# Performance work log

Measured on AMD Instinct MI355X. Metric: run time of the kernel, lower is better.

The kernel has to match this reference:

```python
import jax, jax.numpy as jnp
import numpy as np

N_HEAD, D_MODEL, D_K, D_V = 8, 512, 64, 64
LN_EPS = 1e-3


def setup_inputs() -> dict:
    key = jax.random.key(0)
    ks = jax.random.split(key, 9)
    B, L = 4, 2048
    q = jax.random.normal(ks[0], (B, L, D_MODEL), dtype=jnp.float32)
    k = jax.random.normal(ks[1], (B, L, D_MODEL), dtype=jnp.float32)
    v = jax.random.normal(ks[2], (B, L, D_MODEL), dtype=jnp.float32)
    # xavier-normal-ish init for projections
    s_qk = (2.0 / (D_MODEL + D_K)) ** 0.5
    s_v = (2.0 / (D_MODEL + D_V)) ** 0.5
    s_p = (2.0 / (N_HEAD * D_V + D_MODEL)) ** 0.5
    w_qs = jax.random.normal(ks[3], (N_HEAD, D_MODEL, D_K), dtype=jnp.float32) * s_qk
    w_ks = jax.random.normal(ks[4], (N_HEAD, D_MODEL, D_K), dtype=jnp.float32) * s_qk
    w_vs = jax.random.normal(ks[5], (N_HEAD, D_MODEL, D_V), dtype=jnp.float32) * s_v
    proj_w = jax.random.normal(ks[6], (D_MODEL, N_HEAD * D_V), dtype=jnp.float32) * s_p  # torch Linear weight (out,in)
    proj_b = jnp.zeros((D_MODEL,), dtype=jnp.float32)
    a_2 = jnp.ones((D_MODEL,), dtype=jnp.float32)
    b_2 = jnp.zeros((D_MODEL,), dtype=jnp.float32)
    return {"q": q, "k": k, "v": v, "w_qs": w_qs, "w_ks": w_ks, "w_vs": w_vs,
            "proj_w": proj_w, "proj_b": proj_b, "a_2": a_2, "b_2": b_2}


def _layer_norm(z, a_2, b_2):
    # torch.std default is unbiased (ddof=1); module divides by (sigma + eps)
    mu = jnp.mean(z, axis=-1, keepdims=True)
    sigma = jnp.std(z, axis=-1, keepdims=True, ddof=1)
    return (z - mu) / (sigma + LN_EPS) * a_2 + b_2


def reference(q, k, v, w_qs, w_ks, w_vs, proj_w, proj_b, a_2, b_2):
    B, Lq, D = q.shape
    temper = jnp.asarray(D, q.dtype) ** 0.5  # note: sqrt(d_model), as in source
    residual = q
    # per-head projections: (h, b, l, dk)
    qh = jnp.einsum('bld,hdk->hblk', q, w_qs)
    kh = jnp.einsum('bmd,hdk->hbmk', k, w_ks)
    vh = jnp.einsum('bmd,hdv->hbmv', v, w_vs)
    # full score matrix (h, b, lq, lk) -- faithful to naive bmm attention
    attn = jax.nn.softmax(jnp.einsum('hblk,hbmk->hblm', qh, kh) / temper, axis=-1)
    out = jnp.einsum('hblm,hbmv->hblv', attn, vh)          # (h, b, lq, dv)
    out = jnp.transpose(out, (1, 2, 0, 3)).reshape(B, Lq, -1)  # concat heads -> (b, lq, h*dv)
    out = out @ proj_w.T + proj_b
    out = _layer_norm(out + residual, a_2, b_2)
    attns = attn.reshape(-1, attn.shape[2], attn.shape[3])  # (h*b, lq, lk) matching torch layout
    return out, attns
```

## Files before the change

kernel.cpp:

```cpp
#include <hip/hip_runtime.h>
#include <stdint.h>

typedef unsigned short u16;
typedef u16   u16x4v __attribute__((ext_vector_type(4)));
typedef u16   u16x8v __attribute__((ext_vector_type(8)));
typedef short s16x8v __attribute__((ext_vector_type(8)));
typedef float f32x4v __attribute__((ext_vector_type(4)));

#define DEV static __device__ __forceinline__

DEV u16 f2bf(float f){
  union { float f; unsigned u; } v; v.f = f;
  unsigned r = v.u + 0x7FFFu + ((v.u >> 16) & 1u);
  return (u16)(r >> 16);
}

DEV f32x4v mfma16(s16x8v a, s16x8v b, f32x4v c){
  return __builtin_amdgcn_mfma_f32_16x16x32_bf16(a, b, c, 0, 0, 0);
}

__global__ __launch_bounds__(256) void k_wall(const float* __restrict__ w_qs,
                                              const float* __restrict__ w_ks,
                                              const float* __restrict__ w_vs,
                                              const float* __restrict__ proj_w,
                                              u16* __restrict__ wt, u16* __restrict__ wtp,
                                              float qscale){
  int gid = blockIdx.x;
  int tsel = gid >> 10;
  int e = (gid & 1023) * 256 + threadIdx.x;
  if(tsel == 3){
    wtp[e] = f2bf(proj_w[e]);
  } else {
    const float* w = tsel == 0 ? w_qs : (tsel == 1 ? w_ks : w_vs);
    float sc = tsel == 0 ? qscale : 1.0f;
    int n = e >> 9, d = e & 511;
    int h = n >> 6, kk = n & 63;
    wt[tsel * 262144 + n * 512 + d] = f2bf(w[h * 32768 + d * 64 + kk] * sc);
  }
}

__global__ __launch_bounds__(256) void k_qkv(const float* __restrict__ Q,
                                             const float* __restrict__ K,
                                             const float* __restrict__ V,
                                             const u16* __restrict__ Wt,
                                             u16* __restrict__ qhh, u16* __restrict__ khh,
                                             u16* __restrict__ vtt){
  __shared__ __align__(16) u16 Xs[32 * 520];
  const int t = threadIdx.x;
  const int lane = t & 63, w = t >> 6;
  const int g = lane >> 4, li = lane & 15;
  const int i0 = blockIdx.x * 32;
  const int y = blockIdx.y;
  const int tsel = y >> 1;
  const float* X = tsel == 0 ? Q : (tsel == 1 ? K : V);
  const int n0 = (y & 1) * 256 + w * 64;

  #pragma unroll
  for(int it = 0; it < 16; ++it){
    int s = it * 256 + t, row = s >> 7, c4 = s & 127;
    f32x4v xv = *(const f32x4v*)(X + (size_t)(i0 + row) * 512 + c4 * 4);
    u16x4v bv; bv[0]=f2bf(xv[0]); bv[1]=f2bf(xv[1]); bv[2]=f2bf(xv[2]); bv[3]=f2bf(xv[3]);
    *(u16x4v*)(Xs + row * 520 + c4 * 4) = bv;
  }
  __syncthreads();

  const int wbase = tsel * 512 + n0;
  const u16* wp0 = Wt + (size_t)(wbase +  0 + li) * 512 + g * 8;
  const u16* wp1 = Wt + (size_t)(wbase + 16 + li) * 512 + g * 8;
  const u16* wp2 = Wt + (size_t)(wbase + 32 + li) * 512 + g * 8;
  const u16* wp3 = Wt + (size_t)(wbase + 48 + li) * 512 + g * 8;

#define LOADW(S, c) { \
  S##0 = *(const s16x8v*)(wp0 + (c) * 32); \
  S##1 = *(const s16x8v*)(wp1 + (c) * 32); \
  S##2 = *(const s16x8v*)(wp2 + (c) * 32); \
  S##3 = *(const s16x8v*)(wp3 + (c) * 32); }
#define COMPW(S, c) { \
  int k0 = (c) * 32 + g * 8; \
  s16x8v a0 = *(const s16x8v*)(Xs + li * 520 + k0); \
  s16x8v a1 = *(const s16x8v*)(Xs + (16 + li) * 520 + k0); \
  acc[0][0] = mfma16(a0, S##0, acc[0][0]); acc[1][0] = mfma16(a1, S##0, acc[1][0]); \
  acc[0][1] = mfma16(a0, S##1, acc[0][1]); acc[1][1] = mfma16(a1, S##1, acc[1][1]); \
  acc[0][2] = mfma16(a0, S##2, acc[0][2]); acc[1][2] = mfma16(a1, S##2, acc[1][2]); \
  acc[0][3] = mfma16(a0, S##3, acc[0][3]); acc[1][3] = mfma16(a1, S##3, acc[1][3]); }

  f32x4v acc[2][4] = {};
  s16x8v wA0, wA1, wA2, wA3, wB0, wB1, wB2, wB3;
  LOADW(wA, 0);
  #pragma unroll
  for(int c = 0; c < 16; c += 2){
    LOADW(wB, c + 1);
    COMPW(wA, c);
    if(c + 2 < 16) LOADW(wA, c + 2);
    COMPW(wB, c + 1);
  }
#undef LOADW
#undef COMPW

  if(tsel < 2){
    u16* Y = tsel == 0 ? qhh : khh;
    #pragma unroll
    for(int rg = 0; rg < 2; ++rg)
      #pragma unroll
      for(int j = 0; j < 4; ++j){
        int n = n0 + j * 16 + li, h = n >> 6, dk = n & 63;
        #pragma unroll
        for(int r = 0; r < 4; ++r){
          int i = i0 + rg * 16 + g * 4 + r, bb = i >> 11, m = i & 2047;
          Y[((size_t)(h * 4 + bb) * 2048 + m) * 64 + dk] = f2bf(acc[rg][j][r]);
        }
      }
  } else {
    #pragma unroll
    for(int rg = 0; rg < 2; ++rg)
      #pragma unroll
      for(int j = 0; j < 4; ++j){
        int n = n0 + j * 16 + li;
        u16x4v pk;
        #pragma unroll
        for(int r = 0; r < 4; ++r) pk[r] = f2bf(acc[rg][j][r]);
        *(u16x4v*)(vtt + (size_t)n * 8192 + i0 + g * 8 + rg * 4) = pk;
      }
  }
}


#define LOADK(B, ht) { \
  const u16* _p = kp + (size_t)(ht) * 2048; \
  B##0 = *(const s16x8v*)(_p); \
  B##1 = *(const s16x8v*)(_p + 32); \
  B##2 = *(const s16x8v*)(_p + 1024); \
  B##3 = *(const s16x8v*)(_p + 1056); }

#define STEPA(B) { \
  f32x4v z0 = {}, z1 = {}; \
  z0 = mfma16(B##0, bq00, z0); z0 = mfma16(B##1, bq01, z0); \
  z1 = mfma16(B##2, bq00, z1); z1 = mfma16(B##3, bq01, z1); \
  _Pragma("unroll") for(int r = 0; r < 4; ++r){ s00[r] += exp2f(z0[r]); s01[r] += exp2f(z1[r]); } \
  f32x4v y0 = {}, y1 = {}; \
  y0 = mfma16(B##0, bq10, y0); y0 = mfma16(B##1, bq11, y0); \
  y1 = mfma16(B##2, bq10, y1); y1 = mfma16(B##3, bq11, y1); \
  _Pragma("unroll") for(int r = 0; r < 4; ++r){ s10[r] += exp2f(y0[r]); s11[r] += exp2f(y1[r]); } }

#define LOADV(B, ht) { \
  const u16* _p = vp + (ht) * 32; \
  B##0 = *(const s16x8v*)(_p); \
  B##1 = *(const s16x8v*)(_p + 131072); \
  B##2 = *(const s16x8v*)(_p + 262144); \
  B##3 = *(const s16x8v*)(_p + 393216); }

#define QS_HALF(KB, VB, bqa, bqb, lb, qs_, ht) { \
  f32x4v z0 = {}, z1 = {}; \
  z0 = mfma16(KB##0, bqa, z0); z0 = mfma16(KB##1, bqb, z0); \
  z1 = mfma16(KB##2, bqa, z1); z1 = mfma16(KB##3, bqb, z1); \
  f32x4v p0, p1; \
  _Pragma("unroll") for(int r = 0; r < 4; ++r){ p0[r] = exp2f(z0[r] + lb); p1[r] = exp2f(z1[r] + lb); } \
  float* _ab = attb + (size_t)((qs_) * 16 + li) * 2048 + (ht) * 32 + g * 4; \
  __builtin_nontemporal_store(p0, (f32x4v*)(_ab)); \
  __builtin_nontemporal_store(p1, (f32x4v*)(_ab + 16)); \
  union { u16 hh[8]; s16x8v v; } _u; \
  _Pragma("unroll") for(int r = 0; r < 4; ++r){ _u.hh[r] = f2bf(p0[r]); _u.hh[4 + r] = f2bf(p1[r]); } \
  acc##qs_##0 = mfma16(_u.v, VB##0, acc##qs_##0); \
  acc##qs_##1 = mfma16(_u.v, VB##1, acc##qs_##1); \
  acc##qs_##2 = mfma16(_u.v, VB##2, acc##qs_##2); \
  acc##qs_##3 = mfma16(_u.v, VB##3, acc##qs_##3); }

#define STEPB(KB, VB, ht) { \
  QS_HALF(KB, VB, bq00, bq01, lb0, 0, ht); \
  QS_HALF(KB, VB, bq10, bq11, lb1, 1, ht); }

__global__ __launch_bounds__(256, 3) void k_attn(const u16* __restrict__ QHH, const u16* __restrict__ KHH,
                                                 const u16* __restrict__ VTT,
                                                 u16* __restrict__ XC, float* __restrict__ ATT){
  __shared__ float Lp[2][2][32];
  __shared__ float AccS[2][32][64];
  const int t = threadIdx.x, lane = t & 63, w = t >> 6;
  const int g = lane >> 4, li = lane & 15;
  const int qs = w >> 1, mh = w & 1;
  const int gid = blockIdx.x;
  const int xcd = gid & 7, rem = gid >> 3;
  const int qt = rem & 31;
  const int hb = xcd * 4 + (rem >> 5);
  const int h = hb >> 2, b = hb & 3;
  const size_t base_hb = (size_t)hb * 2048;
  const int qbase = qt * 64 + qs * 32;

  s16x8v bq00, bq01, bq10, bq11;
  {
    const u16* qp0 = QHH + (base_hb + qbase + li) * 64 + g * 8;
    const u16* qp1 = QHH + (base_hb + qbase + 16 + li) * 64 + g * 8;
    bq00 = *(const s16x8v*)(qp0); bq01 = *(const s16x8v*)(qp0 + 32);
    bq10 = *(const s16x8v*)(qp1); bq11 = *(const s16x8v*)(qp1 + 32);
  }
  const u16* kp = KHH + (base_hb + li) * 64 + g * 8 + (size_t)mh * 65536;
  const u16* vp = VTT + (size_t)(h * 64 + li) * 8192 + b * 2048 + g * 8 + mh * 1024;
  float* attb = ATT + (base_hb + qbase) * 2048 + mh * 1024;

  f32x4v s00 = {}, s01 = {}, s10 = {}, s11 = {};
  {
    s16x8v kA0, kA1, kA2, kA3, kB0, kB1, kB2, kB3;
    LOADK(kA, 0);
    for(int ht = 0; ht < 30; ht += 2){
      LOADK(kB, ht + 1);
      STEPA(kA);
      LOADK(kA, ht + 2);
      STEPA(kB);
    }
    LOADK(kB, 31);
    STEPA(kA);
    STEPA(kB);
  }
  float l0 = (s00[0]+s00[1]+s00[2]+s00[3]) + (s01[0]+s01[1]+s01[2]+s01[3]);
  float l1 = (s10[0]+s10[1]+s10[2]+s10[3]) + (s11[0]+s11[1]+s11[2]+s11[3]);
  l0 += __shfl_xor(l0, 16, 64); l0 += __shfl_xor(l0, 32, 64);
  l1 += __shfl_xor(l1, 16, 64); l1 += __shfl_xor(l1, 32, 64);
  if(lane < 16){ Lp[qs][mh][li] = l0; Lp[qs][mh][16 + li] = l1; }
  __syncthreads();
  const float lb0 = -__log2f(Lp[qs][0][li]      + Lp[qs][1][li]);
  const float lb1 = -__log2f(Lp[qs][0][16 + li] + Lp[qs][1][16 + li]);

  f32x4v acc00 = {}, acc01 = {}, acc02 = {}, acc03 = {};
  f32x4v acc10 = {}, acc11 = {}, acc12 = {}, acc13 = {};
  {
    s16x8v kA0, kA1, kA2, kA3, kB0, kB1, kB2, kB3;
    s16x8v vA0, vA1, vA2, vA3, vB0, vB1, vB2, vB3;
    LOADK(kA, 0); LOADV(vA, 0);
    for(int ht = 0; ht < 30; ht += 2){
      LOADK(kB, ht + 1); LOADV(vB, ht + 1);
      STEPB(kA, vA, ht);
      LOADK(kA, ht + 2); LOADV(vA, ht + 2);
      STEPB(kB, vB, ht + 1);
    }
    LOADK(kB, 31); LOADV(vB, 31);
    STEPB(kA, vA, 30);
    STEPB(kB, vB, 31);
  }

  if(mh == 1){
    #pragma unroll
    for(int r = 0; r < 4; ++r){
      AccS[qs][ 0 + r][lane] = acc00[r];
      AccS[qs][ 4 + r][lane] = acc01[r];
      AccS[qs][ 8 + r][lane] = acc02[r];
      AccS[qs][12 + r][lane] = acc03[r];
      AccS[qs][16 + r][lane] = acc10[r];
      AccS[qs][20 + r][lane] = acc11[r];
      AccS[qs][24 + r][lane] = acc12[r];
      AccS[qs][28 + r][lane] = acc13[r];
    }
  }
  __syncthreads();
  if(mh == 0){
    #pragma unroll
    for(int r = 0; r < 4; ++r){
      acc00[r] += AccS[qs][ 0 + r][lane];
      acc01[r] += AccS[qs][ 4 + r][lane];
      acc02[r] += AccS[qs][ 8 + r][lane];
      acc03[r] += AccS[qs][12 + r][lane];
      acc10[r] += AccS[qs][16 + r][lane];
      acc11[r] += AccS[qs][20 + r][lane];
      acc12[r] += AccS[qs][24 + r][lane];
      acc13[r] += AccS[qs][28 + r][lane];
    }
    #pragma unroll
    for(int r = 0; r < 4; ++r){
      int row0 = qbase + g * 4 + r;
      int row1 = qbase + 16 + g * 4 + r;
      u16* x0 = XC + (size_t)(b * 2048 + row0) * 512 + h * 64 + li;
      u16* x1 = XC + (size_t)(b * 2048 + row1) * 512 + h * 64 + li;
      x0[0]  = f2bf(acc00[r]); x0[16] = f2bf(acc01[r]); x0[32] = f2bf(acc02[r]); x0[48] = f2bf(acc03[r]);
      x1[0]  = f2bf(acc10[r]); x1[16] = f2bf(acc11[r]); x1[32] = f2bf(acc12[r]); x1[48] = f2bf(acc13[r]);
    }
  }
}

__global__ __launch_bounds__(512) void k_out(const u16* __restrict__ Xb,
                                             const u16* __restrict__ Wtp,
                                             float* __restrict__ Yf,
                                             const float* __restrict__ bias,
                                             const float* __restrict__ resid,
                                             const float* __restrict__ a2,
                                             const float* __restrict__ b2){
  __shared__ __align__(16) u16 Xs[16 * 520];
  __shared__ float sred[8][16], sqred[8][16], muL[16], rsL[16];
  const int t = threadIdx.x;
  const int lane = t & 63, w = t >> 6;
  const int g = lane >> 4, li = lane & 15;
  const int i0 = blockIdx.x * 16;
  const int n0 = w * 64;

  #pragma unroll
  for(int it = 0; it < 2; ++it){
    int s = it * 512 + t, row = s >> 6, c8 = s & 63;
    u16x8v xv = *(const u16x8v*)(Xb + (size_t)(i0 + row) * 512 + c8 * 8);
    *(u16x8v*)(Xs + row * 520 + c8 * 8) = xv;
  }
  __syncthreads();

  const u16* wp0 = Wtp + (size_t)(n0 +  0 + li) * 512 + g * 8;
  const u16* wp1 = Wtp + (size_t)(n0 + 16 + li) * 512 + g * 8;
  const u16* wp2 = Wtp + (size_t)(n0 + 32 + li) * 512 + g * 8;
  const u16* wp3 = Wtp + (size_t)(n0 + 48 + li) * 512 + g * 8;

#define LOADW(S, c) { \
  S##0 = *(const s16x8v*)(wp0 + (c) * 32); \
  S##1 = *(const s16x8v*)(wp1 + (c) * 32); \
  S##2 = *(const s16x8v*)(wp2 + (c) * 32); \
  S##3 = *(const s16x8v*)(wp3 + (c) * 32); }
#define COMPW(S, c) { \
  int k0 = (c) * 32 + g * 8; \
  s16x8v a0 = *(const s16x8v*)(Xs + li * 520 + k0); \
  acc[0] = mfma16(a0, S##0, acc[0]); \
  acc[1] = mfma16(a0, S##1, acc[1]); \
  acc[2] = mfma16(a0, S##2, acc[2]); \
  acc[3] = mfma16(a0, S##3, acc[3]); }

  f32x4v acc[4] = {};
  s16x8v wA0, wA1, wA2, wA3, wB0, wB1, wB2, wB3;
  LOADW(wA, 0);
  #pragma unroll
  for(int c = 0; c < 16; c += 2){
    LOADW(wB, c + 1);
    COMPW(wA, c);
    if(c + 2 < 16) LOADW(wA, c + 2);
    COMPW(wB, c + 1);
  }
#undef LOADW
#undef COMPW

  float zres[4][4];
  #pragma unroll
  for(int j = 0; j < 4; ++j){
    int n = n0 + j * 16 + li;
    float bv = bias[n];
    #pragma unroll
    for(int r = 0; r < 4; ++r){
      int i = i0 + g * 4 + r;
      zres[j][r] = acc[j][r] + bv + resid[(size_t)i * 512 + n];
    }
  }
  #pragma unroll
  for(int r = 0; r < 4; ++r){
    float S = 0.f, SQ = 0.f;
    #pragma unroll
    for(int j = 0; j < 4; ++j){ float zz = zres[j][r]; S += zz; SQ += zz * zz; }
    #pragma unroll
    for(int off = 1; off < 16; off <<= 1){ S += __shfl_xor(S, off, 16); SQ += __shfl_xor(SQ, off, 16); }
    if(li == 0){ sred[w][g * 4 + r] = S; sqred[w][g * 4 + r] = SQ; }
  }
  __syncthreads();
  if(t < 16){
    float S = 0.f, SQ = 0.f;
    #pragma unroll
    for(int ww = 0; ww < 8; ++ww){ S += sred[ww][t]; SQ += sqred[ww][t]; }
    float mu = S * (1.0f / 512.0f);
    float var = (SQ - 512.0f * mu * mu) * (1.0f / 511.0f);
    muL[t] = mu;
    rsL[t] = 1.0f / (sqrtf(fmaxf(var, 0.0f)) + 1e-3f);
  }
  __syncthreads();
  #pragma unroll
  for(int r = 0; r < 4; ++r){
    int rloc = g * 4 + r;
    float mu = muL[rloc], rs = rsL[rloc];
    size_t ib = (size_t)(i0 + rloc) * 512;
    #pragma unroll
    for(int j = 0; j < 4; ++j){
      int n = n0 + j * 16 + li;
      Yf[ib + n] = (zres[j][r] - mu) * rs * a2[n] + b2[n];
    }
  }
}

extern "C" void kernel_launch(void* const* d_in, const int* in_sizes, int n_in,
                              void* d_out, int out_size, void* d_ws, size_t ws_size,
                              hipStream_t stream){
  const float* q      = (const float*)d_in[0];
  const float* k      = (const float*)d_in[1];
  const float* v      = (const float*)d_in[2];
  const float* w_qs   = (const float*)d_in[3];
  const float* w_ks   = (const float*)d_in[4];
  const float* w_vs   = (const float*)d_in[5];
  const float* proj_w = (const float*)d_in[6];
  const float* proj_b = (const float*)d_in[7];
  const float* a2     = (const float*)d_in[8];
  const float* b2     = (const float*)d_in[9];

  char* ws = (char*)d_ws;
  u16* wt    = (u16*)(ws);
  u16* wtp   = (u16*)(ws + 1572864);
  u16* qhh   = (u16*)(ws + 2097152);
  u16* khh   = (u16*)(ws + 10485760);
  u16* vtt   = (u16*)(ws + 18874368);
  u16* xc    = (u16*)(ws + 27262976);

  float* out = (float*)d_out;
  float* att = out + 4194304;

  const float qscale = 0.06375872032774575f;

  k_wall<<<dim3(4096), 256, 0, stream>>>(w_qs, w_ks, w_vs, proj_w, wt, wtp, qscale);
  k_qkv <<<dim3(256, 6), 256, 0, stream>>>(q, k, v, wt, qhh, khh, vtt);
  k_attn<<<dim3(1024), 256, 0, stream>>>(qhh, khh, vtt, xc, att);
  k_out <<<dim3(512), 512, 0, stream>>>(xc, wtp, out, proj_b, q, a2, b2);
}
```

Measured before the change: 316.7 us.

## Split attention into single-pass PV kernel and separate probability-write kernel

The attention kernel previously made two passes over K: one to compute row sums of exp, and one to recompute scores, write normalized probabilities and accumulate PV. It now accumulates PV with unnormalized exponentials in one pass, normalizes at the end, and stores the log row sums. A new kernel recomputes QK^T and writes the normalized attention matrix with nontemporal stores. This takes the large attention-matrix store out of the PV loop so each kernel has a simpler pipeline. The cost is an extra launch and a second QK^T recomputation. Exponentials are still taken without max subtraction, as before.

After: 378.8 us. +19.6%, slower.

```diff
diff --git a/kernel.cpp b/kernel.cpp
--- a/kernel.cpp
+++ b/kernel.cpp
@@ -132,16 +132,6 @@
   B##2 = *(const s16x8v*)(_p + 1024); \
   B##3 = *(const s16x8v*)(_p + 1056); }
 
-#define STEPA(B) { \
-  f32x4v z0 = {}, z1 = {}; \
-  z0 = mfma16(B##0, bq00, z0); z0 = mfma16(B##1, bq01, z0); \
-  z1 = mfma16(B##2, bq00, z1); z1 = mfma16(B##3, bq01, z1); \
-  _Pragma("unroll") for(int r = 0; r < 4; ++r){ s00[r] += exp2f(z0[r]); s01[r] += exp2f(z1[r]); } \
-  f32x4v y0 = {}, y1 = {}; \
-  y0 = mfma16(B##0, bq10, y0); y0 = mfma16(B##1, bq11, y0); \
-  y1 = mfma16(B##2, bq10, y1); y1 = mfma16(B##3, bq11, y1); \
-  _Pragma("unroll") for(int r = 0; r < 4; ++r){ s10[r] += exp2f(y0[r]); s11[r] += exp2f(y1[r]); } }
-
 #define LOADV(B, ht) { \
   const u16* _p = vp + (ht) * 32; \
   B##0 = *(const s16x8v*)(_p); \
@@ -149,15 +139,13 @@
   B##2 = *(const s16x8v*)(_p + 262144); \
   B##3 = *(const s16x8v*)(_p + 393216); }
 
-#define QS_HALF(KB, VB, bqa, bqb, lb, qs_, ht) { \
+#define PVH(KB, VB, bqa, bqb, qs_, sA, sB) { \
   f32x4v z0 = {}, z1 = {}; \
   z0 = mfma16(KB##0, bqa, z0); z0 = mfma16(KB##1, bqb, z0); \
   z1 = mfma16(KB##2, bqa, z1); z1 = mfma16(KB##3, bqb, z1); \
   f32x4v p0, p1; \
-  _Pragma("unroll") for(int r = 0; r < 4; ++r){ p0[r] = exp2f(z0[r] + lb); p1[r] = exp2f(z1[r] + lb); } \
-  float* _ab = attb + (size_t)((qs_) * 16 + li) * 2048 + (ht) * 32 + g * 4; \
-  __builtin_nontemporal_store(p0, (f32x4v*)(_ab)); \
-  __builtin_nontemporal_store(p1, (f32x4v*)(_ab + 16)); \
+  _Pragma("unroll") for(int r = 0; r < 4; ++r){ p0[r] = exp2f(z0[r]); p1[r] = exp2f(z1[r]); } \
+  _Pragma("unroll") for(int r = 0; r < 4; ++r){ sA[r] += p0[r]; sB[r] += p1[r]; } \
   union { u16 hh[8]; s16x8v v; } _u; \
   _Pragma("unroll") for(int r = 0; r < 4; ++r){ _u.hh[r] = f2bf(p0[r]); _u.hh[4 + r] = f2bf(p1[r]); } \
   acc##qs_##0 = mfma16(_u.v, VB##0, acc##qs_##0); \
@@ -165,13 +153,13 @@
   acc##qs_##2 = mfma16(_u.v, VB##2, acc##qs_##2); \
   acc##qs_##3 = mfma16(_u.v, VB##3, acc##qs_##3); }
 
-#define STEPB(KB, VB, ht) { \
-  QS_HALF(KB, VB, bq00, bq01, lb0, 0, ht); \
-  QS_HALF(KB, VB, bq10, bq11, lb1, 1, ht); }
-
-__global__ __launch_bounds__(256, 3) void k_attn(const u16* __restrict__ QHH, const u16* __restrict__ KHH,
-                                                 const u16* __restrict__ VTT,
-                                                 u16* __restrict__ XC, float* __restrict__ ATT){
+#define PVSTEP(KB, VB) { \
+  PVH(KB, VB, bq00, bq01, 0, s00, s01); \
+  PVH(KB, VB, bq10, bq11, 1, s10, s11); }
+
+__global__ __launch_bounds__(256, 3) void k_pv(const u16* __restrict__ QHH, const u16* __restrict__ KHH,
+                                               const u16* __restrict__ VTT,
+                                               u16* __restrict__ XC, float* __restrict__ LB){
   __shared__ float Lp[2][2][32];
   __shared__ float AccS[2][32][64];
   const int t = threadIdx.x, lane = t & 63, w = t >> 6;
@@ -194,31 +182,8 @@
   }
   const u16* kp = KHH + (base_hb + li) * 64 + g * 8 + (size_t)mh * 65536;
   const u16* vp = VTT + (size_t)(h * 64 + li) * 8192 + b * 2048 + g * 8 + mh * 1024;
-  float* attb = ATT + (base_hb + qbase) * 2048 + mh * 1024;
 
   f32x4v s00 = {}, s01 = {}, s10 = {}, s11 = {};
-  {
-    s16x8v kA0, kA1, kA2, kA3, kB0, kB1, kB2, kB3;
-    LOADK(kA, 0);
-    for(int ht = 0; ht < 30; ht += 2){
-      LOADK(kB, ht + 1);
-      STEPA(kA);
-      LOADK(kA, ht + 2);
-      STEPA(kB);
-    }
-    LOADK(kB, 31);
-    STEPA(kA);
-    STEPA(kB);
-  }
-  float l0 = (s00[0]+s00[1]+s00[2]+s00[3]) + (s01[0]+s01[1]+s01[2]+s01[3]);
-  float l1 = (s10[0]+s10[1]+s10[2]+s10[3]) + (s11[0]+s11[1]+s11[2]+s11[3]);
-  l0 += __shfl_xor(l0, 16, 64); l0 += __shfl_xor(l0, 32, 64);
-  l1 += __shfl_xor(l1, 16, 64); l1 += __shfl_xor(l1, 32, 64);
-  if(lane < 16){ Lp[qs][mh][li] = l0; Lp[qs][mh][16 + li] = l1; }
-  __syncthreads();
-  const float lb0 = -__log2f(Lp[qs][0][li]      + Lp[qs][1][li]);
-  const float lb1 = -__log2f(Lp[qs][0][16 + li] + Lp[qs][1][16 + li]);
-
   f32x4v acc00 = {}, acc01 = {}, acc02 = {}, acc03 = {};
   f32x4v acc10 = {}, acc11 = {}, acc12 = {}, acc13 = {};
   {
@@ -227,15 +192,20 @@
     LOADK(kA, 0); LOADV(vA, 0);
     for(int ht = 0; ht < 30; ht += 2){
       LOADK(kB, ht + 1); LOADV(vB, ht + 1);
-      STEPB(kA, vA, ht);
+      PVSTEP(kA, vA);
       LOADK(kA, ht + 2); LOADV(vA, ht + 2);
-      STEPB(kB, vB, ht + 1);
+      PVSTEP(kB, vB);
     }
     LOADK(kB, 31); LOADV(vB, 31);
-    STEPB(kA, vA, 30);
-    STEPB(kB, vB, 31);
-  }
-
+    PVSTEP(kA, vA);
+    PVSTEP(kB, vB);
+  }
+
+  float l0 = (s00[0]+s00[1]+s00[2]+s00[3]) + (s01[0]+s01[1]+s01[2]+s01[3]);
+  float l1 = (s10[0]+s10[1]+s10[2]+s10[3]) + (s11[0]+s11[1]+s11[2]+s11[3]);
+  l0 += __shfl_xor(l0, 16, 64); l0 += __shfl_xor(l0, 32, 64);
+  l1 += __shfl_xor(l1, 16, 64); l1 += __shfl_xor(l1, 32, 64);
+  if(lane < 16){ Lp[qs][mh][li] = l0; Lp[qs][mh][16 + li] = l1; }
   if(mh == 1){
     #pragma unroll
     for(int r = 0; r < 4; ++r){
@@ -250,17 +220,26 @@
     }
   }
   __syncthreads();
+  if(mh == 0 && lane < 32)
+    LB[base_hb + qbase + lane] = -__log2f(Lp[qs][0][lane] + Lp[qs][1][lane]);
+
   if(mh == 0){
+    float rlA[4], rlB[4];
     #pragma unroll
     for(int r = 0; r < 4; ++r){
-      acc00[r] += AccS[qs][ 0 + r][lane];
-      acc01[r] += AccS[qs][ 4 + r][lane];
-      acc02[r] += AccS[qs][ 8 + r][lane];
-      acc03[r] += AccS[qs][12 + r][lane];
-      acc10[r] += AccS[qs][16 + r][lane];
-      acc11[r] += AccS[qs][20 + r][lane];
-      acc12[r] += AccS[qs][24 + r][lane];
-      acc13[r] += AccS[qs][28 + r][lane];
+      rlA[r] = 1.0f / (Lp[qs][0][g * 4 + r]      + Lp[qs][1][g * 4 + r]);
+      rlB[r] = 1.0f / (Lp[qs][0][16 + g * 4 + r] + Lp[qs][1][16 + g * 4 + r]);
+    }
+    #pragma unroll
+    for(int r = 0; r < 4; ++r){
+      acc00[r] = (acc00[r] + AccS[qs][ 0 + r][lane]) * rlA[r];
+      acc01[r] = (acc01[r] + AccS[qs][ 4 + r][lane]) * rlA[r];
+      acc02[r] = (acc02[r] + AccS[qs][ 8 + r][lane]) * rlA[r];
+      acc03[r] = (acc03[r] + AccS[qs][12 + r][lane]) * rlA[r];
+      acc10[r] = (acc10[r] + AccS[qs][16 + r][lane]) * rlB[r];
+      acc11[r] = (acc11[r] + AccS[qs][20 + r][lane]) * rlB[r];
+      acc12[r] = (acc12[r] + AccS[qs][24 + r][lane]) * rlB[r];
+      acc13[r] = (acc13[r] + AccS[qs][28 + r][lane]) * rlB[r];
     }
     #pragma unroll
     for(int r = 0; r < 4; ++r){
@@ -272,6 +251,63 @@
       x1[0]  = f2bf(acc10[r]); x1[16] = f2bf(acc11[r]); x1[32] = f2bf(acc12[r]); x1[48] = f2bf(acc13[r]);
     }
   }
+}
+
+
+#define LB8(S, s) { \
+  const u16* _p = kp + (size_t)(s) * 2048; \
+  S##0 = *(const s16x8v*)(_p);        S##1 = *(const s16x8v*)(_p + 32); \
+  S##2 = *(const s16x8v*)(_p + 1024); S##3 = *(const s16x8v*)(_p + 1056); \
+  S##4 = *(const s16x8v*)(_p + 2048); S##5 = *(const s16x8v*)(_p + 2080); \
+  S##6 = *(const s16x8v*)(_p + 3072); S##7 = *(const s16x8v*)(_p + 3104); }
+
+#define WSTEP1(A0, A1, A2, A3, ht) { \
+  f32x4v z0 = {}, z1 = {}; \
+  z0 = mfma16(A0, bq0, z0); z0 = mfma16(A1, bq1, z0); \
+  z1 = mfma16(A2, bq0, z1); z1 = mfma16(A3, bq1, z1); \
+  f32x4v p0, p1; \
+  _Pragma("unroll") for(int r = 0; r < 4; ++r){ p0[r] = exp2f(z0[r] + lb); p1[r] = exp2f(z1[r] + lb); } \
+  float* _ab = attb + li * 2048 + (ht) * 32 + g * 4; \
+  __builtin_nontemporal_store(p0, (f32x4v*)(_ab)); \
+  __builtin_nontemporal_store(p1, (f32x4v*)(_ab + 16)); }
+
+#define CS2(S, s) { \
+  WSTEP1(S##0, S##1, S##2, S##3, s); \
+  WSTEP1(S##4, S##5, S##6, S##7, (s) + 1); }
+
+__global__ __launch_bounds__(256, 4) void k_att_write(const u16* __restrict__ QHH,
+                                                      const u16* __restrict__ KHH,
+                                                      const float* __restrict__ LB,
+                                                      float* __restrict__ ATT){
+  const int t = threadIdx.x, lane = t & 63, w = t >> 6;
+  const int g = lane >> 4, li = lane & 15;
+  const int gid = blockIdx.x;
+  const int xcd = gid & 7, rem = gid >> 3;
+  const int qt = rem & 31;
+  const int hb = xcd * 4 + (rem >> 5);
+  const size_t base_hb = (size_t)hb * 2048;
+  const int rowbase = qt * 64 + w * 16;
+
+  s16x8v bq0, bq1;
+  {
+    const u16* qp = QHH + (base_hb + rowbase + li) * 64 + g * 8;
+    bq0 = *(const s16x8v*)(qp); bq1 = *(const s16x8v*)(qp + 32);
+  }
+  const float lb = LB[base_hb + rowbase + li];
+  const u16* kp = KHH + (base_hb + li) * 64 + g * 8;
+  float* attb = ATT + (base_hb + rowbase) * 2048;
+
+  s16x8v kA0, kA1, kA2, kA3, kA4, kA5, kA6, kA7;
+  s16x8v kB0, kB1, kB2, kB3, kB4, kB5, kB6, kB7;
+  LB8(kA, 0); LB8(kB, 2);
+  for(int ht = 0; ht < 60; ht += 4){
+    CS2(kA, ht);
+    LB8(kA, ht + 4);
+    CS2(kB, ht + 2);
+    LB8(kB, ht + 6);
+  }
+  CS2(kA, 60);
+  CS2(kB, 62);
 }
 
 __global__ __launch_bounds__(512) void k_out(const u16* __restrict__ Xb,
@@ -393,14 +429,16 @@
   u16* khh   = (u16*)(ws + 10485760);
   u16* vtt   = (u16*)(ws + 18874368);
   u16* xc    = (u16*)(ws + 27262976);
+  float* lbt = (float*)(ws + 35651584);
 
   float* out = (float*)d_out;
   float* att = out + 4194304;
 
   const float qscale = 0.06375872032774575f;
 
-  k_wall<<<dim3(4096), 256, 0, stream>>>(w_qs, w_ks, w_vs, proj_w, wt, wtp, qscale);
-  k_qkv <<<dim3(256, 6), 256, 0, stream>>>(q, k, v, wt, qhh, khh, vtt);
-  k_attn<<<dim3(1024), 256, 0, stream>>>(qhh, khh, vtt, xc, att);
-  k_out <<<dim3(512), 512, 0, stream>>>(xc, wtp, out, proj_b, q, a2, b2);
-}
+  k_wall     <<<dim3(4096), 256, 0, stream>>>(w_qs, w_ks, w_vs, proj_w, wt, wtp, qscale);
+  k_qkv      <<<dim3(256, 6), 256, 0, stream>>>(q, k, v, wt, qhh, khh, vtt);
+  k_pv       <<<dim3(1024), 256, 0, stream>>>(qhh, khh, vtt, xc, lbt);
+  k_att_write<<<dim3(1024), 256, 0, stream>>>(qhh, khh, lbt, att);
+  k_out      <<<dim3(512), 512, 0, stream>>>(xc, wtp, out, proj_b, q, a2, b2);
+}
```
